# Performance work log

Hardware: AMD Instinct MI355X
Metric: run time of the kernel (lower is better)

## Reference

```python
import jax, jax.numpy as jnp
import numpy as np

B, S, F = 4096, 128, 8
H1, H2 = 64, 32


def setup_inputs() -> dict:
    key = jax.random.key(0)
    ks = jax.random.split(key, 12)
    rn = lambda k, shape, scale: jax.random.normal(k, shape, dtype=jnp.float32) * scale
    return {
        "x": rn(ks[0], (B, S, F), 1.0),
        "time": jax.random.uniform(ks[1], (B, 1), dtype=jnp.float32),
        # linear_combine: (S*F + 1) -> S*F
        "W_combine": rn(ks[2], (S * F, S * F + 1), 1.0 / np.sqrt(S * F + 1)),
        "b_combine": jnp.zeros((S * F,), jnp.float32),
        # LSTM layer 1 (bias=False), gate order i,f,g,o like torch
        "W_ih1": rn(ks[3], (4 * H1, F), 1.0 / np.sqrt(H1)),
        "W_hh1": rn(ks[4], (4 * H1, H1), 1.0 / np.sqrt(H1)),
        # LSTM layer 2 (bias=True)
        "W_ih2": rn(ks[5], (4 * H2, H1), 1.0 / np.sqrt(H2)),
        "W_hh2": rn(ks[6], (4 * H2, H2), 1.0 / np.sqrt(H2)),
        "b_ih2": rn(ks[7], (4 * H2,), 0.05),
        "b_hh2": rn(ks[8], (4 * H2,), 0.05),
        # l_linear_supervised: (H2*S) -> 1
        "W_out": rn(ks[9], (1, H2 * S), 1.0 / np.sqrt(H2 * S)),
        "b_out": jnp.zeros((1,), jnp.float32),
    }


def _lstm(x, W_ih, W_hh, b):
    """batch_first LSTM, zero initial state. x: [B,S,D] -> hidden seq [B,S,H]."""
    Bq = x.shape[0]
    H = W_hh.shape[1]
    # precompute input contribution for all timesteps: [B,S,4H]
    xg = jnp.einsum('bsd,gd->bsg', x, W_ih) + b

    def step(carry, xg_t):
        h, c = carry
        g = xg_t + h @ W_hh.T
        i, f, gg, o = jnp.split(g, 4, axis=-1)  # torch gate order i,f,g,o
        c = jax.nn.sigmoid(f) * c + jax.nn.sigmoid(i) * jnp.tanh(gg)
        h = jax.nn.sigmoid(o) * jnp.tanh(c)
        return (h, c), h

    h0 = jnp.zeros((Bq, H), x.dtype)
    (_, _), hs = jax.lax.scan(step, (h0, h0), jnp.swapaxes(xg, 0, 1))
    return jnp.swapaxes(hs, 0, 1)


def reference(x, time, W_combine, b_combine, W_ih1, W_hh1, W_ih2, W_hh2,
              b_ih2, b_hh2, W_out, b_out):
    Bq = x.shape[0]
    # future_time_as_input == 1 branch: flatten, append time, linear + relu
    xf = jnp.concatenate([x.reshape(Bq, -1), time.reshape(Bq, -1)], axis=1)
    xf = jax.nn.relu(xf @ W_combine.T + b_combine)
    x1 = xf.reshape(Bq, S, F)
    h1 = _lstm(x1, W_ih1, W_hh1, jnp.zeros((4 * H1,), x.dtype))  # [B,S,64]
    h2 = _lstm(h1, W_ih2, W_hh2, b_ih2 + b_hh2)                   # [B,S,32]
    return h2.reshape(Bq, -1) @ W_out.T + b_out                   # [B,1]
```

## Files before the change

kernel.cpp:

```cpp
#include <hip/hip_runtime.h>
#include <math.h>


typedef _Float16 f16x8 __attribute__((ext_vector_type(8)));
typedef float f32x4 __attribute__((ext_vector_type(4)));

union H8 { uint4 q; _Float16 h[8]; f16x8 v; };

#define MF(A, B, C) __builtin_amdgcn_mfma_f32_16x16x32_f16(A, B, C, 0, 0, 0)
#define LOG2E 1.44269504f

__device__ __forceinline__ float sigm_pre(float y) {
  return __builtin_amdgcn_rcpf(1.f + __builtin_amdgcn_exp2f(-y));
}
__device__ __forceinline__ float tanh_raw(float c) {
  return 1.f - 2.f * __builtin_amdgcn_rcpf(1.f + __builtin_amdgcn_exp2f(c * 2.88539008f));
}
__device__ __forceinline__ float lstm_c(float yi, float yf, float yg2, float cold) {
  float Ei = __builtin_amdgcn_exp2f(-yi);
  float Ef = __builtin_amdgcn_exp2f(-yf);
  float Eg = __builtin_amdgcn_exp2f(yg2);
  float Pf = 1.f + Ef;
  float t1 = (1.f + Ei) * (1.f + Eg);
  float num = fmaf(Eg - 1.f, Pf, cold * t1);
  return num * __builtin_amdgcn_rcpf(Pf * t1);
}
__device__ __forceinline__ unsigned pkrtz(float a, float b) {
  return __builtin_bit_cast(unsigned, __builtin_amdgcn_cvt_pkrtz(a, b));
}

__global__ __launch_bounds__(256) void cvt_x(
    const float* __restrict__ x, unsigned* __restrict__ x16)
{
  const int idx = blockIdx.x * 256 + threadIdx.x;
  const float4* src = (const float4*)x;
  float4 a = src[2 * idx], b = src[2 * idx + 1];
  uint4 o = {pkrtz(a.x, a.y), pkrtz(a.z, a.w), pkrtz(b.x, b.y), pkrtz(b.z, b.w)};
  ((uint4*)x16)[idx] = o;
}

#define CROW 72

__global__ __launch_bounds__(256, 2) void combine_mfma(
    const _Float16* __restrict__ xh, const float* __restrict__ tme,
    const float* __restrict__ Wc, const float* __restrict__ bc,
    unsigned* __restrict__ x1u)
{
  __shared__ __align__(16) _Float16 sA[2][128][CROW];
  __shared__ __align__(16) _Float16 sB[2][64][CROW];
  __shared__ float sT[128];
  __shared__ float sWl[64];
  __shared__ float sBc[64];
  _Float16 (*Cst)[CROW] = sA[0];

  const int tid = threadIdx.x;
  const int lane = tid & 63;
  const int w = tid >> 6;
  const int r = lane & 15, grp = lane >> 4;
  const int bid = blockIdx.x;
  const int xcd = bid & 7, j = bid >> 3;
  const int M0 = (xcd * 4 + (j & 3)) * 128;
  const int N0 = (j >> 2) * 64;

  if (tid < 128) sT[tid] = tme[M0 + tid];
  else if (tid < 192) sWl[tid - 128] = Wc[(size_t)(N0 + tid - 128) * 1025 + 1024];
  else sBc[tid - 192] = bc[N0 + tid - 192];

#define STAGE_A(KT, BUF)                                                       \
  _Pragma("unroll") for (int i = 0; i < 4; ++i) {                              \
    int idx = tid + i * 256;                                                   \
    int row = idx >> 3, kq = idx & 7;                                          \
    uint4 v = *(const uint4*)&xh[(size_t)(M0 + row) * 1024 + (KT) + kq * 8];   \
    *(uint4*)&sA[BUF][row][kq * 8] = v;                                        \
  }
#define STAGE_B(KT, BUF)                                                       \
  _Pragma("unroll") for (int i = 0; i < 4; ++i) {                              \
    int idx = tid + i * 256;                                                   \
    int row = idx >> 4, kq = idx & 15;                                         \
    float4 v = *(const float4*)&Wc[(size_t)(N0 + row) * 1025 + (KT) + kq * 4]; \
    *(uint2*)&sB[BUF][row][kq * 4] = uint2{pkrtz(v.x, v.y), pkrtz(v.z, v.w)};  \
  }

  f32x4 acc[2][4];
#pragma unroll
  for (int i = 0; i < 2; ++i)
#pragma unroll
    for (int j2 = 0; j2 < 4; ++j2) acc[i][j2] = f32x4{0.f, 0.f, 0.f, 0.f};

  STAGE_A(0, 0);
  STAGE_B(0, 0);
  __syncthreads();

  int cur = 0;
  for (int kt = 0; kt < 1024; kt += 64) {
    H8 af[2][2], bf[4][2];
#pragma unroll
    for (int i = 0; i < 2; ++i)
#pragma unroll
      for (int c = 0; c < 2; ++c)
        af[i][c].q = *(const uint4*)&sA[cur][w * 32 + i * 16 + r][c * 32 + grp * 8];
#pragma unroll
    for (int j2 = 0; j2 < 4; ++j2)
#pragma unroll
      for (int c = 0; c < 2; ++c)
        bf[j2][c].q = *(const uint4*)&sB[cur][j2 * 16 + r][c * 32 + grp * 8];

    if (kt < 960) {
      STAGE_A(kt + 64, cur ^ 1);
      STAGE_B(kt + 64, cur ^ 1);
    }

#pragma unroll
    for (int i = 0; i < 2; ++i)
#pragma unroll
      for (int j2 = 0; j2 < 4; ++j2) {
        acc[i][j2] = MF(af[i][0].v, bf[j2][0].v, acc[i][j2]);
        acc[i][j2] = MF(af[i][1].v, bf[j2][1].v, acc[i][j2]);
      }
    __syncthreads();
    cur ^= 1;
  }
#undef STAGE_A
#undef STAGE_B

#pragma unroll
  for (int i = 0; i < 2; ++i) {
#pragma unroll
    for (int j2 = 0; j2 < 4; ++j2) {
      int n = j2 * 16 + r;
      float wl = sWl[n], bv = sBc[n];
#pragma unroll
      for (int q = 0; q < 4; ++q) {
        int mm = w * 32 + i * 16 + 4 * grp + q;
        float v = acc[i][j2][q] + sT[mm] * wl + bv;
        Cst[mm][n] = (_Float16)fmaxf(v, 0.f);
      }
    }
  }
  __syncthreads();
#pragma unroll
  for (int i = 0; i < 4; ++i) {
    int idx = tid + i * 256;
    int row = idx >> 3, c8 = idx & 7;
    uint4 v = *(const uint4*)&Cst[row][c8 * 8];
    *(uint4*)&x1u[(size_t)(M0 + row) * 512 + (N0 >> 1) + c8 * 4] = v;
  }
}

#define ROW1 72
#define ROW2 40

__global__ __launch_bounds__(512, 2) void lstm_fused_mfma(
    const unsigned* __restrict__ x1u,
    const float* __restrict__ Wih1, const float* __restrict__ Whh1,
    const float* __restrict__ Wih2, const float* __restrict__ Whh2,
    const float* __restrict__ bih2, const float* __restrict__ bhh2,
    const float* __restrict__ Wout, const float* __restrict__ bout,
    float* __restrict__ out)
{
  __shared__ __align__(16) unsigned sxw[128 * 16 * 4];
  __shared__ float sWoT[32 * 132];
  __shared__ __align__(16) unsigned short sh1[2][16][ROW1];
  __shared__ __align__(16) unsigned short sh2[2][16][ROW2];
  __shared__ float sOut[8][16];

  const int tid = threadIdx.x;
  const int lane = tid & 63;
  const int w = tid >> 6;
  const int vw = w >> 1;
  const int wsub = w & 1;
  const int col = lane & 15;
  const int grp = lane >> 4;
  const int b0 = blockIdx.x * 16;

  const int m1 = col >> 2, g1 = col & 3;
  const float gsc = (g1 == 2) ? 2.f * LOG2E : LOG2E;
  f16x8 A1h[2][2];
  f16x8 A1x[2];
#pragma unroll
  for (int jj = 0; jj < 2; ++jj) {
    const int wr = g1 * 64 + vw * 16 + 4 * m1 + (2 * wsub + jj);
#pragma unroll
    for (int c = 0; c < 2; ++c) {
      H8 f;
#pragma unroll
      for (int q = 0; q < 8; ++q)
        f.h[q] = (_Float16)(Whh1[wr * 64 + c * 32 + grp * 8 + q] * gsc);
      A1h[jj][c] = f.v;
    }
    H8 fx;
#pragma unroll
    for (int q = 0; q < 8; ++q)
      fx.h[q] = (grp == 0) ? (_Float16)(Wih1[wr * 8 + q] * gsc) : (_Float16)0.f;
    A1x[jj] = fx.v;
  }
  f16x8 A2[3];
  const int u = 2 * vw + wsub;
  {
    const int wr = g1 * 32 + 4 * u + m1;
#pragma unroll
    for (int c = 0; c < 3; ++c) {
      H8 f;
#pragma unroll
      for (int q = 0; q < 8; ++q) {
        float wv = (c < 2) ? Wih2[wr * 64 + c * 32 + grp * 8 + q]
                           : Whh2[wr * 32 + grp * 8 + q];
        f.h[q] = (_Float16)(wv * gsc);
      }
      A2[c] = f.v;
    }
  }
  const int h2o = 4 * u + grp;
  f32x4 b2q;
#pragma unroll
  for (int r = 0; r < 4; ++r) {
    const float rs = (r == 2) ? 2.f * LOG2E : LOG2E;
    b2q[r] = (bih2[r * 32 + h2o] + bhh2[r * 32 + h2o]) * rs;
  }
  const f32x4 zq = {0.f, 0.f, 0.f, 0.f};

  for (int idx = tid; idx < 4096; idx += 512) {
    int t = idx >> 5, h = idx & 31;
    sWoT[h * 132 + t] = Wout[idx];
  }
  {
    unsigned short* z = &sh1[0][0][0];
    for (int i2 = tid; i2 < 2 * 16 * ROW1; i2 += 512) z[i2] = 0;
    unsigned short* z2 = &sh2[0][0][0];
    for (int i2 = tid; i2 < 2 * 16 * ROW2; i2 += 512) z2[i2] = 0;
  }
  for (int idx = tid; idx < 16 * 512; idx += 512) {
    int bb = idx >> 9, rem = idx & 511;
    int t = rem >> 2, pr = rem & 3;
    sxw[t * 64 + bb * 4 + pr] = x1u[(size_t)(b0 + bb) * 512 + rem];
  }
  __syncthreads();

  float c1a = 0.f, c1b = 0.f, c2 = 0.f, accO = 0.f;

#define PHASE(T, CUR, DO_L1, DO_L2)                                            \
  {                                                                            \
    H8 s0, s1, s2;                                                             \
    s0.q = *(const uint4*)&sh1[CUR][col][grp * 8];                             \
    s1.q = *(const uint4*)&sh1[CUR][col][32 + grp * 8];                        \
    s2.q = *(const uint4*)&sh2[CUR][col][grp * 8];                             \
    if (DO_L2) {                                                               \
      const float won = sWoT[h2o * 132 + (T) - 1];                             \
      f32x4 a = MF(A2[2], s2.v, b2q);                                          \
      a = MF(A2[0], s0.v, a);                                                  \
      a = MF(A2[1], s1.v, a);                                                  \
      float cc = lstm_c(a[0], a[1], a[2], c2);                                 \
      c2 = cc;                                                                 \
      float hn = sigm_pre(a[3]) * tanh_raw(cc);                                \
      accO = fmaf(hn, won, accO);                                              \
      *(_Float16*)&sh2[(CUR) ^ 1][col][h2o] = (_Float16)hn;                    \
    }                                                                          \
    if (DO_L1) {                                                               \
      H8 sx;                                                                   \
      sx.q = *(const uint4*)&sxw[(T) * 64 + col * 4];                          \
      f32x4 a0 = MF(A1x[0], sx.v, zq);                                         \
      f32x4 a1 = MF(A1x[1], sx.v, zq);                                         \
      a0 = MF(A1h[0][0], s0.v, a0);                                            \
      a1 = MF(A1h[1][0], s0.v, a1);                                            \
      a0 = MF(A1h[0][1], s1.v, a0);                                            \
      a1 = MF(A1h[1][1], s1.v, a1);                                            \
      float cc0 = lstm_c(a0[0], a0[1], a0[2], c1a);                            \
      c1a = cc0;                                                               \
      float h0 = sigm_pre(a0[3]) * tanh_raw(cc0);                              \
      float cc1 = lstm_c(a1[0], a1[1], a1[2], c1b);                            \
      c1b = cc1;                                                               \
      float h1v = sigm_pre(a1[3]) * tanh_raw(cc1);                             \
      *(unsigned*)&sh1[(CUR) ^ 1][col][vw * 16 + 4 * grp + 2 * wsub] =         \
          pkrtz(h0, h1v);                                                      \
    }                                                                          \
    __syncthreads();                                                           \
  }

  PHASE(0, 0, true, false);
  PHASE(1, 1, true, true);
  for (int tt = 1; tt < 64; ++tt) {
    const int t0 = 2 * tt;
    PHASE(t0, 0, true, true);
    PHASE(t0 + 1, 1, true, true);
  }
  PHASE(128, 0, false, true);
#undef PHASE

  accO += __shfl_xor(accO, 16);
  accO += __shfl_xor(accO, 32);
  if (grp == 0) sOut[u][col] = accO;
  __syncthreads();
  if (tid < 16) {
    float s = bout[0];
#pragma unroll
    for (int q = 0; q < 8; ++q) s += sOut[q][tid];
    out[b0 + tid] = s;
  }
}

extern "C" void kernel_launch(void* const* d_in, const int* in_sizes, int n_in,
                              void* d_out, int out_size, void* d_ws, size_t ws_size,
                              hipStream_t stream) {
  const float* x    = (const float*)d_in[0];
  const float* tme  = (const float*)d_in[1];
  const float* Wc   = (const float*)d_in[2];
  const float* bc   = (const float*)d_in[3];
  const float* Wih1 = (const float*)d_in[4];
  const float* Whh1 = (const float*)d_in[5];
  const float* Wih2 = (const float*)d_in[6];
  const float* Whh2 = (const float*)d_in[7];
  const float* bih2 = (const float*)d_in[8];
  const float* bhh2 = (const float*)d_in[9];
  const float* Wout = (const float*)d_in[10];
  const float* bout = (const float*)d_in[11];
  float* outp = (float*)d_out;
  unsigned* x1u = (unsigned*)d_ws;
  unsigned* x16 = x1u + (size_t)4096 * 512;

  cvt_x<<<2048, 256, 0, stream>>>(x, x16);
  combine_mfma<<<512, 256, 0, stream>>>((const _Float16*)x16, tme, Wc, bc, x1u);
  lstm_fused_mfma<<<256, 512, 0, stream>>>(x1u, Wih1, Whh1, Wih2, Whh2,
                                           bih2, bhh2, Wout, bout, outp);
}
```

Baseline: 102.6 us.

## Pre-convert combine weights to fp16 and fuse LSTM hidden activation math

Adds a separate kernel that converts W_combine to fp16 in workspace once per call, so the combine GEMM stages B tiles with 16-byte fp16 loads instead of converting from fp32 inside every block. Combine blocks share W tiles, so this removes repeated fp32 reads and conversions at the cost of an extra launch and a 2 MB write/read. It also merges the sigmoid(o)*tanh(c) computation into one expression with a single reciprocal, shortening the serial recurrence. The fp16 path is only taken when the workspace is large enough, with a fallback to the old path.

```diff
diff --git a/kernel.cpp b/kernel.cpp
--- a/kernel.cpp
+++ b/kernel.cpp
@@ -10,12 +10,6 @@
 #define MF(A, B, C) __builtin_amdgcn_mfma_f32_16x16x32_f16(A, B, C, 0, 0, 0)
 #define LOG2E 1.44269504f
 
-__device__ __forceinline__ float sigm_pre(float y) {
-  return __builtin_amdgcn_rcpf(1.f + __builtin_amdgcn_exp2f(-y));
-}
-__device__ __forceinline__ float tanh_raw(float c) {
-  return 1.f - 2.f * __builtin_amdgcn_rcpf(1.f + __builtin_amdgcn_exp2f(c * 2.88539008f));
-}
 __device__ __forceinline__ float lstm_c(float yi, float yf, float yg2, float cold) {
   float Ei = __builtin_amdgcn_exp2f(-yi);
   float Ef = __builtin_amdgcn_exp2f(-yf);
@@ -25,6 +19,11 @@
   float num = fmaf(Eg - 1.f, Pf, cold * t1);
   return num * __builtin_amdgcn_rcpf(Pf * t1);
 }
+__device__ __forceinline__ float lstm_h(float cc, float yo) {
+  float Ec = __builtin_amdgcn_exp2f(fminf(cc * 2.88539008f, 126.f));
+  float Eo = __builtin_amdgcn_exp2f(-yo);
+  return (Ec - 1.f) * __builtin_amdgcn_rcpf((Ec + 1.f) * (1.f + Eo));
+}
 __device__ __forceinline__ unsigned pkrtz(float a, float b) {
   return __builtin_bit_cast(unsigned, __builtin_amdgcn_cvt_pkrtz(a, b));
 }
@@ -39,12 +38,21 @@
   ((uint4*)x16)[idx] = o;
 }
 
+__global__ __launch_bounds__(256) void cvt_wc(
+    const float* __restrict__ Wc, _Float16* __restrict__ w16)
+{
+  const int gid = blockIdx.x * 256 + threadIdx.x;
+  const int row = gid >> 10, col = gid & 1023;
+  w16[gid] = (_Float16)Wc[(size_t)row * 1025 + col];
+}
+
 #define CROW 72
 
+template <bool W16>
 __global__ __launch_bounds__(256, 2) void combine_mfma(
     const _Float16* __restrict__ xh, const float* __restrict__ tme,
-    const float* __restrict__ Wc, const float* __restrict__ bc,
-    unsigned* __restrict__ x1u)
+    const float* __restrict__ Wc, const _Float16* __restrict__ wch,
+    const float* __restrict__ bc, unsigned* __restrict__ x1u)
 {
   __shared__ __align__(16) _Float16 sA[2][128][CROW];
   __shared__ __align__(16) _Float16 sB[2][64][CROW];
@@ -58,9 +66,9 @@
   const int w = tid >> 6;
   const int r = lane & 15, grp = lane >> 4;
   const int bid = blockIdx.x;
-  const int xcd = bid & 7, j = bid >> 3;
-  const int M0 = (xcd * 4 + (j & 3)) * 128;
-  const int N0 = (j >> 2) * 64;
+  const int xcd = bid & 7, jb = bid >> 3;
+  const int M0 = (xcd * 4 + (jb & 3)) * 128;
+  const int N0 = (jb >> 2) * 64;
 
   if (tid < 128) sT[tid] = tme[M0 + tid];
   else if (tid < 192) sWl[tid - 128] = Wc[(size_t)(N0 + tid - 128) * 1025 + 1024];
@@ -74,11 +82,20 @@
     *(uint4*)&sA[BUF][row][kq * 8] = v;                                        \
   }
 #define STAGE_B(KT, BUF)                                                       \
-  _Pragma("unroll") for (int i = 0; i < 4; ++i) {                              \
-    int idx = tid + i * 256;                                                   \
-    int row = idx >> 4, kq = idx & 15;                                         \
-    float4 v = *(const float4*)&Wc[(size_t)(N0 + row) * 1025 + (KT) + kq * 4]; \
-    *(uint2*)&sB[BUF][row][kq * 4] = uint2{pkrtz(v.x, v.y), pkrtz(v.z, v.w)};  \
+  if (W16) {                                                                   \
+    _Pragma("unroll") for (int i = 0; i < 2; ++i) {                            \
+      int idx = tid + i * 256;                                                 \
+      int row = idx >> 3, kq = idx & 7;                                        \
+      uint4 v = *(const uint4*)&wch[(size_t)(N0 + row) * 1024 + (KT) + kq * 8];\
+      *(uint4*)&sB[BUF][row][kq * 8] = v;                                      \
+    }                                                                          \
+  } else {                                                                     \
+    _Pragma("unroll") for (int i = 0; i < 4; ++i) {                            \
+      int idx = tid + i * 256;                                                 \
+      int row = idx >> 4, kq = idx & 15;                                       \
+      float4 v = *(const float4*)&Wc[(size_t)(N0 + row) * 1025 + (KT) + kq * 4];\
+      *(uint2*)&sB[BUF][row][kq * 4] = uint2{pkrtz(v.x, v.y), pkrtz(v.z, v.w)};\
+    }                                                                          \
   }
 
   f32x4 acc[2][4];
@@ -251,7 +268,7 @@
       a = MF(A2[1], s1.v, a);                                                  \
       float cc = lstm_c(a[0], a[1], a[2], c2);                                 \
       c2 = cc;                                                                 \
-      float hn = sigm_pre(a[3]) * tanh_raw(cc);                                \
+      float hn = lstm_h(cc, a[3]);                                             \
       accO = fmaf(hn, won, accO);                                              \
       *(_Float16*)&sh2[(CUR) ^ 1][col][h2o] = (_Float16)hn;                    \
     }                                                                          \
@@ -266,10 +283,10 @@
       a1 = MF(A1h[1][1], s1.v, a1);                                            \
       float cc0 = lstm_c(a0[0], a0[1], a0[2], c1a);                            \
       c1a = cc0;                                                               \
-      float h0 = sigm_pre(a0[3]) * tanh_raw(cc0);                              \
+      float h0 = lstm_h(cc0, a0[3]);                                           \
       float cc1 = lstm_c(a1[0], a1[1], a1[2], c1b);                            \
       c1b = cc1;                                                               \
-      float h1v = sigm_pre(a1[3]) * tanh_raw(cc1);                             \
+      float h1v = lstm_h(cc1, a1[3]);                                          \
       *(unsigned*)&sh1[(CUR) ^ 1][col][vw * 16 + 4 * grp + 2 * wsub] =         \
           pkrtz(h0, h1v);                                                      \
     }                                                                          \
@@ -316,9 +333,20 @@
   float* outp = (float*)d_out;
   unsigned* x1u = (unsigned*)d_ws;
   unsigned* x16 = x1u + (size_t)4096 * 512;
+  _Float16* wc16 = (_Float16*)(x16 + (size_t)4096 * 512);
+
+  const size_t need = (size_t)4096 * 512 * 4 * 2 + (size_t)1024 * 1024 * 2;
+  const bool useW16 = (ws_size >= need);
 
   cvt_x<<<2048, 256, 0, stream>>>(x, x16);
-  combine_mfma<<<512, 256, 0, stream>>>((const _Float16*)x16, tme, Wc, bc, x1u);
+  if (useW16) {
+    cvt_wc<<<4096, 256, 0, stream>>>(Wc, wc16);
+    combine_mfma<true><<<512, 256, 0, stream>>>((const _Float16*)x16, tme, Wc,
+                                                wc16, bc, x1u);
+  } else {
+    combine_mfma<false><<<512, 256, 0, stream>>>((const _Float16*)x16, tme, Wc,
+                                                 nullptr, bc, x1u);
+  }
   lstm_fused_mfma<<<256, 512, 0, stream>>>(x1u, Wih1, Whh1, Wih2, Whh2,
                                            bih2, bhh2, Wout, bout, outp);
 }
```

Result: no change. 102.3 us (-0.3%).

## Fuse fp32-to-fp16 input conversion into combine GEMM and merge LSTM h activation

Applied to the files above, without the earlier changes.

Drops the separate cvt_x kernel and has the combine GEMM load fp32 x directly, converting to fp16 while staging into shared memory. This removes one launch and a full fp16 copy of x written to and read back from global memory, but each block now reads twice the bytes of A per tile. It also replaces the separate sigmoid(o) and tanh(c) in the LSTM recurrence with one merged expression using a single reciprocal, clamping the exponent to avoid overflow. That shortens the per-step latency on the serial critical path.

```diff
diff --git a/kernel.cpp b/kernel.cpp
--- a/kernel.cpp
+++ b/kernel.cpp
@@ -10,12 +10,6 @@
 #define MF(A, B, C) __builtin_amdgcn_mfma_f32_16x16x32_f16(A, B, C, 0, 0, 0)
 #define LOG2E 1.44269504f
 
-__device__ __forceinline__ float sigm_pre(float y) {
-  return __builtin_amdgcn_rcpf(1.f + __builtin_amdgcn_exp2f(-y));
-}
-__device__ __forceinline__ float tanh_raw(float c) {
-  return 1.f - 2.f * __builtin_amdgcn_rcpf(1.f + __builtin_amdgcn_exp2f(c * 2.88539008f));
-}
 __device__ __forceinline__ float lstm_c(float yi, float yf, float yg2, float cold) {
   float Ei = __builtin_amdgcn_exp2f(-yi);
   float Ef = __builtin_amdgcn_exp2f(-yf);
@@ -25,24 +19,19 @@
   float num = fmaf(Eg - 1.f, Pf, cold * t1);
   return num * __builtin_amdgcn_rcpf(Pf * t1);
 }
+__device__ __forceinline__ float lstm_h(float cc, float yo) {
+  float Ec = __builtin_amdgcn_exp2f(fminf(cc * 2.88539008f, 126.f));
+  float Eo = __builtin_amdgcn_exp2f(-yo);
+  return (Ec - 1.f) * __builtin_amdgcn_rcpf((Ec + 1.f) * (1.f + Eo));
+}
 __device__ __forceinline__ unsigned pkrtz(float a, float b) {
   return __builtin_bit_cast(unsigned, __builtin_amdgcn_cvt_pkrtz(a, b));
 }
 
-__global__ __launch_bounds__(256) void cvt_x(
-    const float* __restrict__ x, unsigned* __restrict__ x16)
-{
-  const int idx = blockIdx.x * 256 + threadIdx.x;
-  const float4* src = (const float4*)x;
-  float4 a = src[2 * idx], b = src[2 * idx + 1];
-  uint4 o = {pkrtz(a.x, a.y), pkrtz(a.z, a.w), pkrtz(b.x, b.y), pkrtz(b.z, b.w)};
-  ((uint4*)x16)[idx] = o;
-}
-
 #define CROW 72
 
 __global__ __launch_bounds__(256, 2) void combine_mfma(
-    const _Float16* __restrict__ xh, const float* __restrict__ tme,
+    const float* __restrict__ x, const float* __restrict__ tme,
     const float* __restrict__ Wc, const float* __restrict__ bc,
     unsigned* __restrict__ x1u)
 {
@@ -58,20 +47,20 @@
   const int w = tid >> 6;
   const int r = lane & 15, grp = lane >> 4;
   const int bid = blockIdx.x;
-  const int xcd = bid & 7, j = bid >> 3;
-  const int M0 = (xcd * 4 + (j & 3)) * 128;
-  const int N0 = (j >> 2) * 64;
+  const int xcd = bid & 7, jb = bid >> 3;
+  const int M0 = (xcd * 4 + (jb & 3)) * 128;
+  const int N0 = (jb >> 2) * 64;
 
   if (tid < 128) sT[tid] = tme[M0 + tid];
   else if (tid < 192) sWl[tid - 128] = Wc[(size_t)(N0 + tid - 128) * 1025 + 1024];
   else sBc[tid - 192] = bc[N0 + tid - 192];
 
 #define STAGE_A(KT, BUF)                                                       \
-  _Pragma("unroll") for (int i = 0; i < 4; ++i) {                              \
+  _Pragma("unroll") for (int i = 0; i < 8; ++i) {                              \
     int idx = tid + i * 256;                                                   \
-    int row = idx >> 3, kq = idx & 7;                                          \
-    uint4 v = *(const uint4*)&xh[(size_t)(M0 + row) * 1024 + (KT) + kq * 8];   \
-    *(uint4*)&sA[BUF][row][kq * 8] = v;                                        \
+    int row = idx >> 4, kq = idx & 15;                                         \
+    float4 v = *(const float4*)&x[(size_t)(M0 + row) * 1024 + (KT) + kq * 4];  \
+    *(uint2*)&sA[BUF][row][kq * 4] = uint2{pkrtz(v.x, v.y), pkrtz(v.z, v.w)};  \
   }
 #define STAGE_B(KT, BUF)                                                       \
   _Pragma("unroll") for (int i = 0; i < 4; ++i) {                              \
@@ -251,7 +240,7 @@
       a = MF(A2[1], s1.v, a);                                                  \
       float cc = lstm_c(a[0], a[1], a[2], c2);                                 \
       c2 = cc;                                                                 \
-      float hn = sigm_pre(a[3]) * tanh_raw(cc);                                \
+      float hn = lstm_h(cc, a[3]);                                             \
       accO = fmaf(hn, won, accO);                                              \
       *(_Float16*)&sh2[(CUR) ^ 1][col][h2o] = (_Float16)hn;                    \
     }                                                                          \
@@ -266,10 +255,10 @@
       a1 = MF(A1h[1][1], s1.v, a1);                                            \
       float cc0 = lstm_c(a0[0], a0[1], a0[2], c1a);                            \
       c1a = cc0;                                                               \
-      float h0 = sigm_pre(a0[3]) * tanh_raw(cc0);                              \
+      float h0 = lstm_h(cc0, a0[3]);                                           \
       float cc1 = lstm_c(a1[0], a1[1], a1[2], c1b);                            \
       c1b = cc1;                                                               \
-      float h1v = sigm_pre(a1[3]) * tanh_raw(cc1);                             \
+      float h1v = lstm_h(cc1, a1[3]);                                          \
       *(unsigned*)&sh1[(CUR) ^ 1][col][vw * 16 + 4 * grp + 2 * wsub] =         \
           pkrtz(h0, h1v);                                                      \
     }                                                                          \
@@ -315,10 +304,8 @@
   const float* bout = (const float*)d_in[11];
   float* outp = (float*)d_out;
   unsigned* x1u = (unsigned*)d_ws;
-  unsigned* x16 = x1u + (size_t)4096 * 512;
-
-  cvt_x<<<2048, 256, 0, stream>>>(x, x16);
-  combine_mfma<<<512, 256, 0, stream>>>((const _Float16*)x16, tme, Wc, bc, x1u);
+
+  combine_mfma<<<512, 256, 0, stream>>>(x, tme, Wc, bc, x1u);
   lstm_fused_mfma<<<256, 512, 0, stream>>>(x1u, Wih1, Whh1, Wih2, Whh2,
                                            bih2, bhh2, Wout, bout, outp);
 }
```

Result: faster. 98.50 us (-4.0%).
